# Performance work log

Hardware: AMD Instinct MI355X
Metric: run time of the kernel (lower is better)

The kernel has to match this reference:

```python
import jax, jax.numpy as jnp
import numpy as np
import math

INPUT_SZ = 512
HIDDEN_SZ = 1024


def setup_inputs() -> dict:
    key = jax.random.key(0)
    ks = jax.random.split(key, 13)
    stdv = 1.0 / math.sqrt(HIDDEN_SZ)

    def u(k, shape):
        return jax.random.uniform(k, shape, jnp.float32, -stdv, stdv)

    x = jax.random.normal(ks[0], (32, 512, INPUT_SZ), jnp.float32)
    names = ['f', 'i', 'o', 'g']
    inp = {'x': x}
    ki = 1
    for n in names:
        inp[f'U_{n}'] = u(ks[ki], (INPUT_SZ, HIDDEN_SZ)); ki += 1
        inp[f'V_{n}'] = u(ks[ki], (HIDDEN_SZ, HIDDEN_SZ)); ki += 1
        inp[f'b_{n}'] = u(ks[ki], (HIDDEN_SZ,)); ki += 1
    return inp


def reference(x, U_f, V_f, b_f, U_i, V_i, b_i, U_o, V_o, b_o, U_g, V_g, b_g):
    bs, seq_sz, _ = x.shape
    hid = V_f.shape[0]
    # Precompute all input projections for the 4 gates in one pass (parallel over time).
    U = jnp.concatenate([U_f, U_i, U_o, U_g], axis=1)        # [in, 4H]
    V = jnp.concatenate([V_f, V_i, V_o, V_g], axis=1)        # [H, 4H]
    b = jnp.concatenate([b_f, b_i, b_o, b_g], axis=0)        # [4H]
    xU = jnp.einsum('bti,ih->bth', x, U) + b                 # [bs, T, 4H]

    def step(carry, xu_t):
        h_t, c_t = carry
        gates = xu_t + h_t @ V                               # [bs, 4H]
        f_t = jax.nn.sigmoid(gates[:, 0 * hid:1 * hid])
        i_t = jax.nn.sigmoid(gates[:, 1 * hid:2 * hid])
        o_t = jax.nn.sigmoid(gates[:, 2 * hid:3 * hid])
        g_t = jnp.tanh(gates[:, 3 * hid:4 * hid])
        c_t = f_t * c_t + i_t * g_t
        h_t = o_t * jnp.tanh(c_t)
        return (h_t, c_t), h_t

    h0 = jnp.zeros((bs, hid), x.dtype)
    c0 = jnp.zeros((bs, hid), x.dtype)
    (h_last, _), hs = jax.lax.scan(step, (h0, c0), jnp.swapaxes(xU, 0, 1))
    hidden_seq = jnp.swapaxes(hs, 0, 1)                      # [bs, T, H]
    return h_last, hidden_seq
```

## Files before the change

### kernel.cpp

```cpp
#include <hip/hip_runtime.h>


typedef __bf16 bf16x8 __attribute__((ext_vector_type(8)));
typedef float f32x16 __attribute__((ext_vector_type(16)));

#define NWG 64
#define T_STEPS 512
#define HID 1024
#define BS 32
#define WS_RING 59768832
#define WS_FULL 126877696

__device__ __forceinline__ unsigned short f2bf(float f) {
  unsigned int u = __float_as_uint(f);
  u = (u + 0x7FFFu + ((u >> 16) & 1u)) >> 16;
  return (unsigned short)u;
}
__device__ __forceinline__ float b2f(unsigned short s) {
  return __uint_as_float(((unsigned int)s) << 16);
}
__device__ __forceinline__ float sigm(float v) {
  v = fminf(fmaxf(v, -30.f), 30.f);
  return 1.f / (1.f + __expf(-v));
}
__device__ __forceinline__ float tanh_(float v) {
  v = fminf(fmaxf(v, -15.f), 15.f);
  float e = __expf(-2.f * v);
  return (1.f - e) / (1.f + e);
}

__global__ void cvt_x_kernel(const float* __restrict__ x,
                             unsigned int* __restrict__ xfH,
                             unsigned int* __restrict__ xfL) {
  const int t = blockIdx.x;
  const int tid = threadIdx.x;
  __shared__ float xs[32 * 512];
  {
    const int b = tid >> 3;
    const int k0 = (tid & 7) * 64;
    const float* src = x + ((size_t)(b * 512 + t)) * 512 + k0;
    for (int i = 0; i < 64; i += 4) {
      float4 v = *reinterpret_cast<const float4*>(src + i);
      xs[b * 512 + k0 + i + 0] = v.x;
      xs[b * 512 + k0 + i + 1] = v.y;
      xs[b * 512 + k0 + i + 2] = v.z;
      xs[b * 512 + k0 + i + 3] = v.w;
    }
  }
  __syncthreads();
  unsigned int* dH = xfH + (size_t)t * 8192;
  unsigned int* dL = xfL + (size_t)t * 8192;
  for (int i = 0; i < 32; ++i) {
    int idx = i * 256 + tid;
    int kt = idx >> 8;
    int pos = idx & 255;
    int lane = pos >> 2;
    int r = pos & 3;
    int kk = 8 * (lane >> 5) + 2 * r;
    int b2 = lane & 31;
    float f0 = xs[b2 * 512 + kt * 16 + kk];
    float f1 = xs[b2 * 512 + kt * 16 + kk + 1];
    unsigned short h0 = f2bf(f0), h1 = f2bf(f1);
    unsigned short l0 = f2bf(f0 - b2f(h0)), l1 = f2bf(f1 - b2f(h1));
    dH[idx] = (unsigned int)h0 | ((unsigned int)h1 << 16);
    dL[idx] = (unsigned int)l0 | ((unsigned int)l1 << 16);
  }
}

__global__ void cvt_uv_kernel(const float* Uf, const float* Vf,
                              const float* Ui, const float* Vi,
                              const float* Uo, const float* Vo,
                              const float* Ug, const float* Vg,
                              unsigned int* __restrict__ vfH,
                              unsigned int* __restrict__ vfL,
                              unsigned int* __restrict__ ufH,
                              unsigned int* __restrict__ ufL) {
  int blk = blockIdx.x;
  int kt = blk % 96;
  int nt = (blk / 96) & 1;
  int wg = blk / 192;
  int lane = threadIdx.x;
  int col32 = lane & 31;
  int c64 = nt * 32 + col32;
  int gate = c64 >> 4;
  int jg = wg * 16 + (c64 & 15);
  const float* V_ = (gate == 0) ? Vf : (gate == 1) ? Vi : (gate == 2) ? Vo : Vg;
  const float* U_ = (gate == 0) ? Uf : (gate == 1) ? Ui : (gate == 2) ? Uo : Ug;
  for (int r = 0; r < 4; ++r) {
    int kk = 8 * (lane >> 5) + 2 * r;
    if (kt < 64) {
      int K = kt * 16 + kk;
      float f0 = V_[(size_t)K * HID + jg];
      float f1 = V_[(size_t)(K + 1) * HID + jg];
      unsigned short h0 = f2bf(f0), h1 = f2bf(f1);
      unsigned short l0 = f2bf(f0 - b2f(h0)), l1 = f2bf(f1 - b2f(h1));
      size_t idx = ((size_t)(wg * 2 + nt) * 64 + kt) * 256 + lane * 4 + r;
      vfH[idx] = (unsigned int)h0 | ((unsigned int)h1 << 16);
      vfL[idx] = (unsigned int)l0 | ((unsigned int)l1 << 16);
    } else {
      int K = (kt - 64) * 16 + kk;
      float f0 = U_[(size_t)K * HID + jg];
      float f1 = U_[(size_t)(K + 1) * HID + jg];
      unsigned short h0 = f2bf(f0), h1 = f2bf(f1);
      unsigned short l0 = f2bf(f0 - b2f(h0)), l1 = f2bf(f1 - b2f(h1));
      size_t idx = ((size_t)(wg * 2 + nt) * 32 + (kt - 64)) * 256 + lane * 4 + r;
      ufH[idx] = (unsigned int)h0 | ((unsigned int)h1 << 16);
      ufL[idx] = (unsigned int)l0 | ((unsigned int)l1 << 16);
    }
  }
}

__device__ __forceinline__ int gidx(int nt, int w, int row, int col) {
  return ((nt * 8 + w) * 32 + row) * 32 + (col ^ row);
}

template <int FULLSEQ>
__global__ __launch_bounds__(512, 2) void lstm_main(
    const unsigned short* __restrict__ ufragH,
    const unsigned short* __restrict__ ufragL,
    const unsigned short* __restrict__ vfragH,
    const unsigned short* __restrict__ vfragL,
    const unsigned short* __restrict__ xfragH,
    const unsigned short* __restrict__ xfragL,
    unsigned int* hfH, unsigned int* hfL, unsigned int* flags,
    const float* __restrict__ bfv, const float* __restrict__ biv,
    const float* __restrict__ bov, const float* __restrict__ bgv,
    float* __restrict__ out) {
  __shared__ unsigned short ldsU[2 * 32 * 512];
  __shared__ float gbuf[2 * 8 * 32 * 32];
  __shared__ float hcell[32][17];

  const int wg = blockIdx.x;
  const int tid = threadIdx.x;
  const int lane = tid & 63;
  const int w = tid >> 6;

  {
    const bf16x8* src = reinterpret_cast<const bf16x8*>(ufragH + (size_t)wg * 32768);
    bf16x8* dst = reinterpret_cast<bf16x8*>(ldsU);
    for (int i = 0; i < 8; ++i) dst[i * 512 + tid] = src[i * 512 + tid];
  }
  __syncthreads();
  __builtin_amdgcn_fence(__ATOMIC_ACQUIRE, "agent");

  bf16x8 uL[2][4], vH[2][8], vL[2][8];
#pragma unroll
  for (int nt = 0; nt < 2; ++nt) {
    const bf16x8* bl = reinterpret_cast<const bf16x8*>(ufragL + (size_t)wg * 32768) +
                       (size_t)nt * 32 * 64;
#pragma unroll
    for (int p = 0; p < 4; ++p) uL[nt][p] = bl[(w * 4 + p) * 64 + lane];
    const bf16x8* vh =
        reinterpret_cast<const bf16x8*>(vfragH + (size_t)((wg * 2 + nt) * 64) * 512);
    const bf16x8* vl =
        reinterpret_cast<const bf16x8*>(vfragL + (size_t)((wg * 2 + nt) * 64) * 512);
#pragma unroll
    for (int q = 0; q < 8; ++q) {
      vH[nt][q] = vh[(w * 8 + q) * 64 + lane];
      vL[nt][q] = vl[(w * 8 + q) * 64 + lane];
    }
  }

  const int b_ = tid & 31;
  const int jp_ = (tid >> 5) & 7;
  const int jg0 = wg * 16 + 2 * jp_;
  const float Bf0 = bfv[jg0], Bf1 = bfv[jg0 + 1];
  const float Bi0 = biv[jg0], Bi1 = biv[jg0 + 1];
  const float Bo0 = bov[jg0], Bo1 = bov[jg0 + 1];
  const float Bg0 = bgv[jg0], Bg1 = bgv[jg0 + 1];
  float c0 = 0.f, c1 = 0.f;
  const int hw = wg * 256 + (b_ + 32 * (jp_ >> 2)) * 4 + (jp_ & 3);

#pragma unroll 1
  for (int t = 0; t < T_STEPS; ++t) {
    f32x16 acc0 = {};
    f32x16 acc1 = {};

    {
      const bf16x8* axh = reinterpret_cast<const bf16x8*>(xfragH + (size_t)t * 16384);
      const bf16x8* axl = reinterpret_cast<const bf16x8*>(xfragL + (size_t)t * 16384);
      const bf16x8* lu = reinterpret_cast<const bf16x8*>(ldsU);
#pragma unroll
      for (int p = 0; p < 4; ++p) {
        int ktx = w * 4 + p;
        bf16x8 ah = axh[ktx * 64 + lane];
        bf16x8 al = axl[ktx * 64 + lane];
        bf16x8 u0 = lu[ktx * 64 + lane];
        bf16x8 u1 = lu[(32 + ktx) * 64 + lane];
        acc0 = __builtin_amdgcn_mfma_f32_32x32x16_bf16(ah, u0, acc0, 0, 0, 0);
        acc0 = __builtin_amdgcn_mfma_f32_32x32x16_bf16(ah, uL[0][p], acc0, 0, 0, 0);
        acc0 = __builtin_amdgcn_mfma_f32_32x32x16_bf16(al, u0, acc0, 0, 0, 0);
        acc1 = __builtin_amdgcn_mfma_f32_32x32x16_bf16(ah, u1, acc1, 0, 0, 0);
        acc1 = __builtin_amdgcn_mfma_f32_32x32x16_bf16(ah, uL[1][p], acc1, 0, 0, 0);
        acc1 = __builtin_amdgcn_mfma_f32_32x32x16_bf16(al, u1, acc1, 0, 0, 0);
      }
    }

    if (t > 0) {
      if (tid < NWG) {
        while (__hip_atomic_load(&flags[tid], __ATOMIC_RELAXED,
                                 __HIP_MEMORY_SCOPE_AGENT) < (unsigned int)t) {
        }
      }
      __syncthreads();
      if (FULLSEQ) {
        const bf16x8* ahh = reinterpret_cast<const bf16x8*>(
            reinterpret_cast<const unsigned short*>(hfH) + (size_t)(t - 1) * 32768);
        const bf16x8* ahl = reinterpret_cast<const bf16x8*>(
            reinterpret_cast<const unsigned short*>(hfL) + (size_t)(t - 1) * 32768);
        bf16x8 aH[8], aL[8];
#pragma unroll
        for (int q = 0; q < 8; ++q) {
          aH[q] = ahh[(w * 8 + q) * 64 + lane];
          aL[q] = ahl[(w * 8 + q) * 64 + lane];
        }
#pragma unroll
        for (int q = 0; q < 8; ++q) {
          acc0 = __builtin_amdgcn_mfma_f32_32x32x16_bf16(aH[q], vH[0][q], acc0, 0, 0, 0);
          acc0 = __builtin_amdgcn_mfma_f32_32x32x16_bf16(aH[q], vL[0][q], acc0, 0, 0, 0);
          acc0 = __builtin_amdgcn_mfma_f32_32x32x16_bf16(aL[q], vH[0][q], acc0, 0, 0, 0);
          acc1 = __builtin_amdgcn_mfma_f32_32x32x16_bf16(aH[q], vH[1][q], acc1, 0, 0, 0);
          acc1 = __builtin_amdgcn_mfma_f32_32x32x16_bf16(aH[q], vL[1][q], acc1, 0, 0, 0);
          acc1 = __builtin_amdgcn_mfma_f32_32x32x16_bf16(aL[q], vH[1][q], acc1, 0, 0, 0);
        }
      } else {
        const unsigned int* hbH = hfH + (size_t)((t - 1) & 3) * 16384 + lane * 4;
        const unsigned int* hbL = hfL + (size_t)((t - 1) & 3) * 16384 + lane * 4;
        unsigned int rH[32], rL[32];
#pragma unroll
        for (int q = 0; q < 8; ++q)
#pragma unroll
          for (int d = 0; d < 4; ++d) {
            rH[q * 4 + d] = __hip_atomic_load(hbH + (w * 8 + q) * 256 + d,
                                              __ATOMIC_RELAXED,
                                              __HIP_MEMORY_SCOPE_AGENT);
            rL[q * 4 + d] = __hip_atomic_load(hbL + (w * 8 + q) * 256 + d,
                                              __ATOMIC_RELAXED,
                                              __HIP_MEMORY_SCOPE_AGENT);
          }
#pragma unroll
        for (int q = 0; q < 8; ++q) {
          union { unsigned int u[4]; bf16x8 v; } aH, aL;
#pragma unroll
          for (int d = 0; d < 4; ++d) {
            aH.u[d] = rH[q * 4 + d];
            aL.u[d] = rL[q * 4 + d];
          }
          acc0 = __builtin_amdgcn_mfma_f32_32x32x16_bf16(aH.v, vH[0][q], acc0, 0, 0, 0);
          acc0 = __builtin_amdgcn_mfma_f32_32x32x16_bf16(aH.v, vL[0][q], acc0, 0, 0, 0);
          acc0 = __builtin_amdgcn_mfma_f32_32x32x16_bf16(aL.v, vH[0][q], acc0, 0, 0, 0);
          acc1 = __builtin_amdgcn_mfma_f32_32x32x16_bf16(aH.v, vH[1][q], acc1, 0, 0, 0);
          acc1 = __builtin_amdgcn_mfma_f32_32x32x16_bf16(aH.v, vL[1][q], acc1, 0, 0, 0);
          acc1 = __builtin_amdgcn_mfma_f32_32x32x16_bf16(aL.v, vH[1][q], acc1, 0, 0, 0);
        }
      }
    }

    {
      const int colw = lane & 31;
      const int rbase = 4 * (lane >> 5);
#pragma unroll
      for (int r = 0; r < 16; ++r) {
        int row = (r & 3) + 8 * (r >> 2) + rbase;
        gbuf[gidx(0, w, row, colw)] = acc0[r];
        gbuf[gidx(1, w, row, colw)] = acc1[r];
      }
    }
    __syncthreads();

    if (tid < 256) {
      const int jl0 = 2 * jp_, jl1 = jl0 + 1;
      float gf0 = Bf0, gf1 = Bf1, gi0 = Bi0, gi1 = Bi1;
      float go0 = Bo0, go1 = Bo1, gg0 = Bg0, gg1 = Bg1;
#pragma unroll
      for (int ww = 0; ww < 8; ++ww) {
        gf0 += gbuf[gidx(0, ww, b_, jl0)];
        gf1 += gbuf[gidx(0, ww, b_, jl1)];
        gi0 += gbuf[gidx(0, ww, b_, 16 + jl0)];
        gi1 += gbuf[gidx(0, ww, b_, 16 + jl1)];
        go0 += gbuf[gidx(1, ww, b_, jl0)];
        go1 += gbuf[gidx(1, ww, b_, jl1)];
        gg0 += gbuf[gidx(1, ww, b_, 16 + jl0)];
        gg1 += gbuf[gidx(1, ww, b_, 16 + jl1)];
      }
      c0 = sigm(gf0) * c0 + sigm(gi0) * tanh_(gg0);
      c1 = sigm(gf1) * c1 + sigm(gi1) * tanh_(gg1);
      float h0 = sigm(go0) * tanh_(c0);
      float h1 = sigm(go1) * tanh_(c1);
      hcell[b_][jl0] = h0;
      hcell[b_][jl1] = h1;
      unsigned short h0h = f2bf(h0), h1h = f2bf(h1);
      unsigned short h0l = f2bf(h0 - b2f(h0h)), h1l = f2bf(h1 - b2f(h1h));
      unsigned int hvH = (unsigned int)h0h | ((unsigned int)h1h << 16);
      unsigned int hvL = (unsigned int)h0l | ((unsigned int)h1l << 16);
      size_t slotbase = FULLSEQ ? (size_t)t * 16384 : (size_t)(t & 3) * 16384;
      __hip_atomic_store(&hfH[slotbase + hw], hvH, __ATOMIC_RELAXED,
                         __HIP_MEMORY_SCOPE_AGENT);
      __hip_atomic_store(&hfL[slotbase + hw], hvL, __ATOMIC_RELAXED,
                         __HIP_MEMORY_SCOPE_AGENT);
    }
    __syncthreads();
    if (tid == 0) {
      __hip_atomic_store(&flags[wg], (unsigned int)(t + 1), __ATOMIC_RELAXED,
                         __HIP_MEMORY_SCOPE_AGENT);
    }
    {
      const int b2 = tid >> 4, jj = tid & 15;
      float hv = hcell[b2][jj];
      __builtin_nontemporal_store(
          hv, out + 32768 + ((size_t)(b2 * T_STEPS + t)) * HID + wg * 16 + jj);
      if (t == T_STEPS - 1)
        __builtin_nontemporal_store(hv, out + (size_t)b2 * HID + wg * 16 + jj);
    }
  }
}

__global__ __launch_bounds__(256) void r9_step_gemm(
    const float* __restrict__ x, const float* __restrict__ hbuf,
    const float* __restrict__ Vf, const float* __restrict__ Vi,
    const float* __restrict__ Vo, const float* __restrict__ Vg,
    const float* __restrict__ Uf, const float* __restrict__ Ui,
    const float* __restrict__ Uo, const float* __restrict__ Ug,
    float* __restrict__ P, int t) {
  const int kb = blockIdx.x;
  const int cb = blockIdx.y;
  const int tidx = threadIdx.x;
  const int gate = cb >> 2;
  const int j = (cb & 3) * 256 + tidx;
  const int col = cb * 256 + tidx;
  const float* V_ = (gate == 0) ? Vf : (gate == 1) ? Vi : (gate == 2) ? Vo : Vg;
  const float* U_ = (gate == 0) ? Uf : (gate == 1) ? Ui : (gate == 2) ? Uo : Ug;
  __shared__ float hs[BS][32];
  __shared__ float xs2[BS][32];
  {
    int idx = tidx * 4;
#pragma unroll
    for (int i = 0; i < 4; ++i, ++idx) {
      int b = idx >> 5, u = idx & 31;
      hs[b][u] = hbuf[b * HID + kb * 32 + u];
      if (kb < 16) xs2[b][u] = x[((size_t)b * T_STEPS + t) * 512 + kb * 32 + u];
    }
  }
  __syncthreads();
  float acc[BS];
#pragma unroll
  for (int b = 0; b < BS; ++b) acc[b] = 0.f;
  const float* vp = V_ + (size_t)(kb * 32) * HID + j;
#pragma unroll 4
  for (int k = 0; k < 32; ++k) {
    float vv = vp[(size_t)k * HID];
#pragma unroll
    for (int b = 0; b < BS; ++b) acc[b] += hs[b][k] * vv;
  }
  if (kb < 16) {
    const float* up = U_ + (size_t)(kb * 32) * HID + j;
#pragma unroll 4
    for (int k = 0; k < 32; ++k) {
      float uv = up[(size_t)k * HID];
#pragma unroll
      for (int b = 0; b < BS; ++b) acc[b] += xs2[b][k] * uv;
    }
  }
  float* pp = P + (size_t)kb * BS * 4096 + col;
#pragma unroll
  for (int b = 0; b < BS; ++b) pp[(size_t)b * 4096] = acc[b];
}

__global__ __launch_bounds__(256) void r9_step_cell(
    const float* __restrict__ P,
    const float* __restrict__ bfv, const float* __restrict__ biv,
    const float* __restrict__ bov, const float* __restrict__ bgv,
    float* __restrict__ hbuf, float* __restrict__ cbuf,
    float* __restrict__ out, int t) {
  const int idx = blockIdx.x * 256 + threadIdx.x;
  const int b = idx >> 10, j = idx & 1023;
  float gf = bfv[j], gi = biv[j], go = bov[j], gg = bgv[j];
  const float* pb = P + (size_t)b * 4096;
#pragma unroll 8
  for (int kb = 0; kb < 32; ++kb) {
    const float* pk = pb + (size_t)kb * BS * 4096;
    gf += pk[j];
    gi += pk[1024 + j];
    go += pk[2048 + j];
    gg += pk[3072 + j];
  }
  float fs = sigm(gf), is = sigm(gi), os = sigm(go), gt = tanh_(gg);
  float c = fs * cbuf[idx] + is * gt;
  cbuf[idx] = c;
  float h = os * tanh_(c);
  hbuf[idx] = h;
  out[32768 + ((size_t)b * T_STEPS + t) * HID + j] = h;
  if (t == T_STEPS - 1) out[(size_t)b * HID + j] = h;
}

extern "C" void kernel_launch(void* const* d_in, const int* in_sizes, int n_in,
                              void* d_out, int out_size, void* d_ws, size_t ws_size,
                              hipStream_t stream) {
  const float *x, *Uf, *Vf, *bf, *Ui, *Vi, *bi, *Uo, *Vo, *bo, *Ug, *Vg, *bg;
  float* out = (float*)d_out;

  bool okA = (n_in == 13) && in_sizes[0] == 8388608 && in_sizes[1] == 524288 &&
             in_sizes[2] == 1048576 && in_sizes[3] == 1024 &&
             in_sizes[4] == 524288 && in_sizes[7] == 524288 &&
             in_sizes[10] == 524288 && in_sizes[12] == 1024;
  if (okA) {
    x = (const float*)d_in[0];
    Uf = (const float*)d_in[1];  Vf = (const float*)d_in[2];  bf = (const float*)d_in[3];
    Ui = (const float*)d_in[4];  Vi = (const float*)d_in[5];  bi = (const float*)d_in[6];
    Uo = (const float*)d_in[7];  Vo = (const float*)d_in[8];  bo = (const float*)d_in[9];
    Ug = (const float*)d_in[10]; Vg = (const float*)d_in[11]; bg = (const float*)d_in[12];
  } else {
    Uf = (const float*)d_in[0];  Ug = (const float*)d_in[1];
    Ui = (const float*)d_in[2];  Uo = (const float*)d_in[3];
    Vf = (const float*)d_in[4];  Vg = (const float*)d_in[5];
    Vi = (const float*)d_in[6];  Vo = (const float*)d_in[7];
    bf = (const float*)d_in[8];  bg = (const float*)d_in[9];
    bi = (const float*)d_in[10]; bo = (const float*)d_in[11];
    x = (const float*)d_in[12];
  }

  char* ws = (char*)d_ws;
  if (ws_size >= (size_t)WS_RING) {
    unsigned int* flags = (unsigned int*)(ws + 0);
    unsigned int* vfragH = (unsigned int*)(ws + 1048576);
    unsigned int* vfragL = (unsigned int*)(ws + 9437184);
    unsigned int* ufragH = (unsigned int*)(ws + 17825792);
    unsigned int* ufragL = (unsigned int*)(ws + 22020096);
    unsigned int* xfragH = (unsigned int*)(ws + 26214400);
    unsigned int* xfragL = (unsigned int*)(ws + 42991616);
    const bool full = ws_size >= (size_t)WS_FULL;
    unsigned int* hfH = (unsigned int*)(full ? ws + 59768832 : ws + 65536);
    unsigned int* hfL = (unsigned int*)(full ? ws + 93323264 : ws + 327680);

    (void)hipMemsetAsync(flags, 0, 4096, stream);
    cvt_uv_kernel<<<64 * 2 * 96, 64, 0, stream>>>(Uf, Vf, Ui, Vi, Uo, Vo, Ug, Vg,
                                                  vfragH, vfragL, ufragH, ufragL);
    cvt_x_kernel<<<512, 256, 0, stream>>>(x, xfragH, xfragL);
    if (full) {
      lstm_main<1><<<NWG, 512, 0, stream>>>(
          (unsigned short*)ufragH, (unsigned short*)ufragL, (unsigned short*)vfragH,
          (unsigned short*)vfragL, (unsigned short*)xfragH, (unsigned short*)xfragL,
          hfH, hfL, flags, bf, bi, bo, bg, out);
    } else {
      lstm_main<0><<<NWG, 512, 0, stream>>>(
          (unsigned short*)ufragH, (unsigned short*)ufragL, (unsigned short*)vfragH,
          (unsigned short*)vfragL, (unsigned short*)xfragH, (unsigned short*)xfragL,
          hfH, hfL, flags, bf, bi, bo, bg, out);
    }
  } else {
    float* P = (float*)ws;
    float* hbuf = (float*)(ws + 16777216);
    float* cbuf = (float*)(ws + 16908288);
    (void)hipMemsetAsync(hbuf, 0, 131072, stream);
    (void)hipMemsetAsync(cbuf, 0, 131072, stream);
    for (int t = 0; t < T_STEPS; ++t) {
      r9_step_gemm<<<dim3(32, 16), 256, 0, stream>>>(x, hbuf, Vf, Vi, Vo, Vg, Uf, Ui,
                                                     Uo, Ug, P, t);
      r9_step_cell<<<128, 256, 0, stream>>>(P, bf, bi, bo, bg, hbuf, cbuf, out, t);
    }
  }
}
```

Baseline: 3.888 ms.

## Move fp32 output writes out of recurrent loop into separate expand kernel

The recurrent kernel no longer writes fp32 hidden states through an LDS transpose buffer each step. It stores only the bf16 hi/lo split of h into a full-sequence workspace, and a new expand_out kernel rebuilds fp32 outputs afterwards. The per-step spin-wait is spread across all waves (each polls 8 flags) and the block barrier after the wait is dropped. The cell-thread mapping is changed so stores are contiguous per thread id. The ring-buffer fallback is removed, so the fast path now requires the full workspace. Output is now the sum of the bf16 hi and lo parts rather than the exact fp32 h, which adds a small rounding difference.

After: 5.008 ms. 28.8% more time.

```diff
diff --git a/kernel.cpp b/kernel.cpp
--- a/kernel.cpp
+++ b/kernel.cpp
@@ -8,7 +8,6 @@
 #define T_STEPS 512
 #define HID 1024
 #define BS 32
-#define WS_RING 59768832
 #define WS_FULL 126877696
 
 __device__ __forceinline__ unsigned short f2bf(float f) {
@@ -114,7 +113,6 @@
   return ((nt * 8 + w) * 32 + row) * 32 + (col ^ row);
 }
 
-template <int FULLSEQ>
 __global__ __launch_bounds__(512, 2) void lstm_main(
     const unsigned short* __restrict__ ufragH,
     const unsigned short* __restrict__ ufragL,
@@ -124,11 +122,9 @@
     const unsigned short* __restrict__ xfragL,
     unsigned int* hfH, unsigned int* hfL, unsigned int* flags,
     const float* __restrict__ bfv, const float* __restrict__ biv,
-    const float* __restrict__ bov, const float* __restrict__ bgv,
-    float* __restrict__ out) {
+    const float* __restrict__ bov, const float* __restrict__ bgv) {
   __shared__ unsigned short ldsU[2 * 32 * 512];
   __shared__ float gbuf[2 * 8 * 32 * 32];
-  __shared__ float hcell[32][17];
 
   const int wg = blockIdx.x;
   const int tid = threadIdx.x;
@@ -161,15 +157,14 @@
     }
   }
 
-  const int b_ = tid & 31;
-  const int jp_ = (tid >> 5) & 7;
+  const int b_ = (tid >> 2) & 31;
+  const int jp_ = ((tid >> 7) & 1) * 4 + (tid & 3);
   const int jg0 = wg * 16 + 2 * jp_;
   const float Bf0 = bfv[jg0], Bf1 = bfv[jg0 + 1];
   const float Bi0 = biv[jg0], Bi1 = biv[jg0 + 1];
   const float Bo0 = bov[jg0], Bo1 = bov[jg0 + 1];
   const float Bg0 = bgv[jg0], Bg1 = bgv[jg0 + 1];
   float c0 = 0.f, c1 = 0.f;
-  const int hw = wg * 256 + (b_ + 32 * (jp_ >> 2)) * 4 + (jp_ & 3);
 
 #pragma unroll 1
   for (int t = 0; t < T_STEPS; ++t) {
@@ -197,62 +192,29 @@
     }
 
     if (t > 0) {
-      if (tid < NWG) {
-        while (__hip_atomic_load(&flags[tid], __ATOMIC_RELAXED,
+      if (lane < 8) {
+        while (__hip_atomic_load(&flags[w * 8 + lane], __ATOMIC_RELAXED,
                                  __HIP_MEMORY_SCOPE_AGENT) < (unsigned int)t) {
         }
       }
-      __syncthreads();
-      if (FULLSEQ) {
-        const bf16x8* ahh = reinterpret_cast<const bf16x8*>(
-            reinterpret_cast<const unsigned short*>(hfH) + (size_t)(t - 1) * 32768);
-        const bf16x8* ahl = reinterpret_cast<const bf16x8*>(
-            reinterpret_cast<const unsigned short*>(hfL) + (size_t)(t - 1) * 32768);
-        bf16x8 aH[8], aL[8];
-#pragma unroll
-        for (int q = 0; q < 8; ++q) {
-          aH[q] = ahh[(w * 8 + q) * 64 + lane];
-          aL[q] = ahl[(w * 8 + q) * 64 + lane];
-        }
-#pragma unroll
-        for (int q = 0; q < 8; ++q) {
-          acc0 = __builtin_amdgcn_mfma_f32_32x32x16_bf16(aH[q], vH[0][q], acc0, 0, 0, 0);
-          acc0 = __builtin_amdgcn_mfma_f32_32x32x16_bf16(aH[q], vL[0][q], acc0, 0, 0, 0);
-          acc0 = __builtin_amdgcn_mfma_f32_32x32x16_bf16(aL[q], vH[0][q], acc0, 0, 0, 0);
-          acc1 = __builtin_amdgcn_mfma_f32_32x32x16_bf16(aH[q], vH[1][q], acc1, 0, 0, 0);
-          acc1 = __builtin_amdgcn_mfma_f32_32x32x16_bf16(aH[q], vL[1][q], acc1, 0, 0, 0);
-          acc1 = __builtin_amdgcn_mfma_f32_32x32x16_bf16(aL[q], vH[1][q], acc1, 0, 0, 0);
-        }
-      } else {
-        const unsigned int* hbH = hfH + (size_t)((t - 1) & 3) * 16384 + lane * 4;
-        const unsigned int* hbL = hfL + (size_t)((t - 1) & 3) * 16384 + lane * 4;
-        unsigned int rH[32], rL[32];
-#pragma unroll
-        for (int q = 0; q < 8; ++q)
-#pragma unroll
-          for (int d = 0; d < 4; ++d) {
-            rH[q * 4 + d] = __hip_atomic_load(hbH + (w * 8 + q) * 256 + d,
-                                              __ATOMIC_RELAXED,
-                                              __HIP_MEMORY_SCOPE_AGENT);
-            rL[q * 4 + d] = __hip_atomic_load(hbL + (w * 8 + q) * 256 + d,
-                                              __ATOMIC_RELAXED,
-                                              __HIP_MEMORY_SCOPE_AGENT);
-          }
-#pragma unroll
-        for (int q = 0; q < 8; ++q) {
-          union { unsigned int u[4]; bf16x8 v; } aH, aL;
-#pragma unroll
-          for (int d = 0; d < 4; ++d) {
-            aH.u[d] = rH[q * 4 + d];
-            aL.u[d] = rL[q * 4 + d];
-          }
-          acc0 = __builtin_amdgcn_mfma_f32_32x32x16_bf16(aH.v, vH[0][q], acc0, 0, 0, 0);
-          acc0 = __builtin_amdgcn_mfma_f32_32x32x16_bf16(aH.v, vL[0][q], acc0, 0, 0, 0);
-          acc0 = __builtin_amdgcn_mfma_f32_32x32x16_bf16(aL.v, vH[0][q], acc0, 0, 0, 0);
-          acc1 = __builtin_amdgcn_mfma_f32_32x32x16_bf16(aH.v, vH[1][q], acc1, 0, 0, 0);
-          acc1 = __builtin_amdgcn_mfma_f32_32x32x16_bf16(aH.v, vL[1][q], acc1, 0, 0, 0);
-          acc1 = __builtin_amdgcn_mfma_f32_32x32x16_bf16(aL.v, vH[1][q], acc1, 0, 0, 0);
-        }
+      const bf16x8* ahh = reinterpret_cast<const bf16x8*>(
+          reinterpret_cast<const unsigned short*>(hfH) + (size_t)(t - 1) * 32768);
+      const bf16x8* ahl = reinterpret_cast<const bf16x8*>(
+          reinterpret_cast<const unsigned short*>(hfL) + (size_t)(t - 1) * 32768);
+      bf16x8 aH[8], aL[8];
+#pragma unroll
+      for (int q = 0; q < 8; ++q) {
+        aH[q] = ahh[(w * 8 + q) * 64 + lane];
+        aL[q] = ahl[(w * 8 + q) * 64 + lane];
+      }
+#pragma unroll
+      for (int q = 0; q < 8; ++q) {
+        acc0 = __builtin_amdgcn_mfma_f32_32x32x16_bf16(aH[q], vH[0][q], acc0, 0, 0, 0);
+        acc0 = __builtin_amdgcn_mfma_f32_32x32x16_bf16(aH[q], vL[0][q], acc0, 0, 0, 0);
+        acc0 = __builtin_amdgcn_mfma_f32_32x32x16_bf16(aL[q], vH[0][q], acc0, 0, 0, 0);
+        acc1 = __builtin_amdgcn_mfma_f32_32x32x16_bf16(aH[q], vH[1][q], acc1, 0, 0, 0);
+        acc1 = __builtin_amdgcn_mfma_f32_32x32x16_bf16(aH[q], vL[1][q], acc1, 0, 0, 0);
+        acc1 = __builtin_amdgcn_mfma_f32_32x32x16_bf16(aL[q], vH[1][q], acc1, 0, 0, 0);
       }
     }
 
@@ -287,16 +249,14 @@
       c1 = sigm(gf1) * c1 + sigm(gi1) * tanh_(gg1);
       float h0 = sigm(go0) * tanh_(c0);
       float h1 = sigm(go1) * tanh_(c1);
-      hcell[b_][jl0] = h0;
-      hcell[b_][jl1] = h1;
       unsigned short h0h = f2bf(h0), h1h = f2bf(h1);
       unsigned short h0l = f2bf(h0 - b2f(h0h)), h1l = f2bf(h1 - b2f(h1h));
       unsigned int hvH = (unsigned int)h0h | ((unsigned int)h1h << 16);
       unsigned int hvL = (unsigned int)h0l | ((unsigned int)h1l << 16);
-      size_t slotbase = FULLSEQ ? (size_t)t * 16384 : (size_t)(t & 3) * 16384;
-      __hip_atomic_store(&hfH[slotbase + hw], hvH, __ATOMIC_RELAXED,
+      size_t base = (size_t)t * 16384 + wg * 256 + tid;
+      __hip_atomic_store(&hfH[base], hvH, __ATOMIC_RELAXED,
                          __HIP_MEMORY_SCOPE_AGENT);
-      __hip_atomic_store(&hfL[slotbase + hw], hvL, __ATOMIC_RELAXED,
+      __hip_atomic_store(&hfL[base], hvL, __ATOMIC_RELAXED,
                          __HIP_MEMORY_SCOPE_AGENT);
     }
     __syncthreads();
@@ -304,13 +264,36 @@
       __hip_atomic_store(&flags[wg], (unsigned int)(t + 1), __ATOMIC_RELAXED,
                          __HIP_MEMORY_SCOPE_AGENT);
     }
-    {
-      const int b2 = tid >> 4, jj = tid & 15;
-      float hv = hcell[b2][jj];
-      __builtin_nontemporal_store(
-          hv, out + 32768 + ((size_t)(b2 * T_STEPS + t)) * HID + wg * 16 + jj);
-      if (t == T_STEPS - 1)
-        __builtin_nontemporal_store(hv, out + (size_t)b2 * HID + wg * 16 + jj);
+  }
+}
+
+__global__ __launch_bounds__(256) void expand_out(
+    const unsigned int* __restrict__ hfH, const unsigned int* __restrict__ hfL,
+    float* __restrict__ out) {
+  if (blockIdx.x == 0 && threadIdx.x == 0) {
+  }
+  __builtin_amdgcn_fence(__ATOMIC_ACQUIRE, "agent");
+  const int tid = threadIdx.x;
+#pragma unroll
+  for (int i = 0; i < 4; ++i) {
+    size_t g = (size_t)blockIdx.x * 1024 + i * 256 + tid;
+    int t = (int)(g >> 14);
+    int d = (int)(g & 16383);
+    int wg = d >> 8;
+    int off = d & 255;
+    int lane_h = off >> 2;
+    int r_h = off & 3;
+    int b = lane_h & 31;
+    int jp = (lane_h >> 5) * 4 + r_h;
+    int j0 = wg * 16 + 2 * jp;
+    unsigned int uH = hfH[g];
+    unsigned int uL = hfL[g];
+    float f0 = b2f((unsigned short)(uH & 0xFFFF)) + b2f((unsigned short)(uL & 0xFFFF));
+    float f1 = b2f((unsigned short)(uH >> 16)) + b2f((unsigned short)(uL >> 16));
+    float2 v = make_float2(f0, f1);
+    *reinterpret_cast<float2*>(out + 32768 + ((size_t)(b * T_STEPS + t)) * HID + j0) = v;
+    if (t == T_STEPS - 1) {
+      *reinterpret_cast<float2*>(out + (size_t)b * HID + j0) = v;
     }
   }
 }
@@ -420,7 +403,7 @@
   }
 
   char* ws = (char*)d_ws;
-  if (ws_size >= (size_t)WS_RING) {
+  if (ws_size >= (size_t)WS_FULL) {
     unsigned int* flags = (unsigned int*)(ws + 0);
     unsigned int* vfragH = (unsigned int*)(ws + 1048576);
     unsigned int* vfragL = (unsigned int*)(ws + 9437184);
@@ -428,25 +411,18 @@
     unsigned int* ufragL = (unsigned int*)(ws + 22020096);
     unsigned int* xfragH = (unsigned int*)(ws + 26214400);
     unsigned int* xfragL = (unsigned int*)(ws + 42991616);
-    const bool full = ws_size >= (size_t)WS_FULL;
-    unsigned int* hfH = (unsigned int*)(full ? ws + 59768832 : ws + 65536);
-    unsigned int* hfL = (unsigned int*)(full ? ws + 93323264 : ws + 327680);
+    unsigned int* hfH = (unsigned int*)(ws + 59768832);
+    unsigned int* hfL = (unsigned int*)(ws + 93323264);
 
     (void)hipMemsetAsync(flags, 0, 4096, stream);
     cvt_uv_kernel<<<64 * 2 * 96, 64, 0, stream>>>(Uf, Vf, Ui, Vi, Uo, Vo, Ug, Vg,
                                                   vfragH, vfragL, ufragH, ufragL);
     cvt_x_kernel<<<512, 256, 0, stream>>>(x, xfragH, xfragL);
-    if (full) {
-      lstm_main<1><<<NWG, 512, 0, stream>>>(
-          (unsigned short*)ufragH, (unsigned short*)ufragL, (unsigned short*)vfragH,
-          (unsigned short*)vfragL, (unsigned short*)xfragH, (unsigned short*)xfragL,
-          hfH, hfL, flags, bf, bi, bo, bg, out);
-    } else {
-      lstm_main<0><<<NWG, 512, 0, stream>>>(
-          (unsigned short*)ufragH, (unsigned short*)ufragL, (unsigned short*)vfragH,
-          (unsigned short*)vfragL, (unsigned short*)xfragH, (unsigned short*)xfragL,
-          hfH, hfL, flags, bf, bi, bo, bg, out);
-    }
+    lstm_main<<<NWG, 512, 0, stream>>>(
+        (unsigned short*)ufragH, (unsigned short*)ufragL, (unsigned short*)vfragH,
+        (unsigned short*)vfragL, (unsigned short*)xfragH, (unsigned short*)xfragL,
+        hfH, hfL, flags, bf, bi, bo, bg);
+    expand_out<<<8192, 256, 0, stream>>>(hfH, hfL, out);
   } else {
     float* P = (float*)ws;
     float* hbuf = (float*)(ws + 16777216);
```
